# Performance work log

Measured on AMD Instinct MI355X. Metric: run time of the kernel, lower is better.

## Reference

```python
import jax, jax.numpy as jnp
import numpy as np

V = 50000
E = 640000
DIM = 128
NUM_EDGE_TYPES = 32


def setup_inputs() -> dict:
    key = jax.random.key(0)
    ks = jax.random.split(key, 8)
    return {
        "node_values": jax.random.normal(ks[0], (V, DIM), dtype=jnp.float32),
        "edge_src": jax.random.randint(ks[1], (E,), 0, V, dtype=jnp.int32),
        "edge_dest": jax.random.randint(ks[2], (E,), 0, V, dtype=jnp.int32),
        "edge_cls": jax.random.randint(ks[3], (E,), 0, NUM_EDGE_TYPES, dtype=jnp.int32),
        "W_src": jax.random.normal(ks[4], (DIM, DIM), dtype=jnp.float32) / np.sqrt(DIM),
        "b_src": jnp.zeros((DIM,), dtype=jnp.float32),
        "W_dest": jax.random.normal(ks[5], (DIM, DIM), dtype=jnp.float32) / np.sqrt(DIM),
        "b_dest": jnp.zeros((DIM,), dtype=jnp.float32),
        "edge_emb": jax.random.normal(ks[6], (NUM_EDGE_TYPES, DIM), dtype=jnp.float32),
    }


def reference(node_values, edge_src, edge_dest, edge_cls, W_src, b_src, W_dest, b_dest, edge_emb):
    # Dense projections over all nodes, then gather per edge (matches tf.gather(dense(...), idx))
    src_proj = node_values @ W_src + b_src    # [V, dim]
    dest_proj = node_values @ W_dest + b_dest  # [V, dim]
    # Per-edge fused message: gather src, gather dest, edge-class embedding lookup, add, relu
    msgs = jax.nn.relu(src_proj[edge_src] + dest_proj[edge_dest] + edge_emb[edge_cls])  # [E, dim]
    # Scatter-reduce messages onto destination nodes
    out = jax.ops.segment_sum(msgs, edge_dest, num_segments=V)  # [V, dim]
    return out
```

## Files before the change

### kernel.cpp

```cpp
#include <hip/hip_runtime.h>


#define V 50000
#define E 640000
#define DIM 128
#define NXCD 8
#define DRANGE 6250
#define NBIN_R 50
#define BINW 125
#define BINCAP 2048
#define NCHUNK 256
#define EC4 625
#define NE_MAX 512
#define QCAP 384
#define NPROJ 782

typedef __bf16 bf16x8 __attribute__((ext_vector_type(8)));
typedef float  f32x4  __attribute__((ext_vector_type(4)));
typedef float  f32x2  __attribute__((ext_vector_type(2)));

__device__ __forceinline__ float bf2f(unsigned int u16) {
    union { unsigned int i; float f; } c; c.i = u16 << 16; return c.f;
}
__device__ __forceinline__ unsigned int f2bf(float f) {
    union { float f; unsigned int i; } c; c.f = f;
    unsigned int u = c.i;
    return (u + 0x7FFFu + ((u >> 16) & 1u)) >> 16;
}

__global__ __launch_bounds__(256) void mp_setup(
    const float* __restrict__ Ws, const float* __restrict__ Wd,
    const float* __restrict__ emb,
    unsigned short* __restrict__ Wpk, unsigned short* __restrict__ embB,
    int* __restrict__ binCnt)
{
    int tid = blockIdx.x * 256 + threadIdx.x;
    int mat  = tid >> 11;
    int rem  = tid & 2047;
    int ct   = rem >> 8;
    int kt   = (rem >> 6) & 3;
    int lane = rem & 63;
    const float* W = mat ? Wd : Ws;
    int n  = ct * 16 + (lane & 15);
    int k0 = kt * 32 + (lane >> 4) * 8;
    unsigned short* dst = Wpk + (size_t)tid * 8;
    #pragma unroll
    for (int j = 0; j < 8; ++j) dst[j] = (unsigned short)f2bf(W[(k0 + j) * DIM + n]);
    embB[tid] = (unsigned short)f2bf(emb[tid]);
    if (tid < NXCD * NBIN_R) binCnt[tid] = 0;
}

__global__ __launch_bounds__(256) void mp_fused(
    const int* __restrict__ ed, const int* __restrict__ es, const int* __restrict__ ec,
    int* __restrict__ binCnt, int* __restrict__ binbuf,
    const float* __restrict__ x, const unsigned short* __restrict__ Wpk,
    const float* __restrict__ bs, const float* __restrict__ bd,
    unsigned char* __restrict__ ps8, unsigned short* __restrict__ pdB)
{
    __shared__ int ebuf[NE_MAX];
    __shared__ unsigned char bbin[NE_MAX];
    __shared__ int csr[NE_MAX];
    __shared__ unsigned char sbin[NE_MAX];
    __shared__ int hist[NBIN_R];
    __shared__ int lofs[NBIN_R + 1];
    __shared__ int lcur[NBIN_R];
    __shared__ int gbase[NBIN_R];
    __shared__ int ecnt;
    __shared__ float stage[4][16 * 132];

    const int b = blockIdx.x;
    const int role = b % 3;
    const int t = threadIdx.x;

    if (role != 2) {
        const int chunk = (b / 3) * 2 + role;
        const int r = chunk & (NXCD - 1);
        const int c = chunk >> 3;
        const int dlo = r * DRANGE;

        if (t < NBIN_R) hist[t] = 0;
        if (t == 0) ecnt = 0;
        __syncthreads();

        int4 DV[3], SV[3], CV[3];
        {
            const int4* ed4 = (const int4*)ed + c * EC4;
            const int4* es4 = (const int4*)es + c * EC4;
            const int4* ec4 = (const int4*)ec + c * EC4;
            #pragma unroll
            for (int k = 0; k < 3; ++k) {
                int i = t + k * 256;
                if (i < EC4) { DV[k] = ed4[i]; SV[k] = es4[i]; CV[k] = ec4[i]; }
                else { DV[k] = make_int4(-1, -1, -1, -1);
                       SV[k] = make_int4(0, 0, 0, 0); CV[k] = make_int4(0, 0, 0, 0); }
            }
        }

        #pragma unroll
        for (int k = 0; k < 3; ++k) {
            #define PUSH(D, S, C) { \
                int rel = (D) - dlo; \
                if ((unsigned)rel < DRANGE) { \
                    int bin = (unsigned)rel / BINW; \
                    int rl  = rel - bin * BINW; \
                    atomicAdd(&hist[bin], 1); \
                    int pos = atomicAdd(&ecnt, 1); \
                    if (pos < NE_MAX) { \
                        ebuf[pos] = ((S) & 0xFFFF) | ((C) << 16) | (rl << 21); \
                        bbin[pos] = (unsigned char)bin; \
                    } } }
            PUSH(DV[k].x, SV[k].x, CV[k].x); PUSH(DV[k].y, SV[k].y, CV[k].y);
            PUSH(DV[k].z, SV[k].z, CV[k].z); PUSH(DV[k].w, SV[k].w, CV[k].w);
            #undef PUSH
        }
        __syncthreads();

        if (t < NBIN_R) gbase[t] = atomicAdd(&binCnt[r * NBIN_R + t], hist[t]);
        if (t < 64) {
            int v = (t < NBIN_R) ? hist[t] : 0;
            #pragma unroll
            for (int dlt = 1; dlt < 64; dlt <<= 1) {
                int u = __shfl_up(v, dlt, 64);
                if (t >= dlt) v += u;
            }
            if (t < NBIN_R) { lofs[t + 1] = v; lcur[t] = v - hist[t]; }
            if (t == 0) lofs[0] = 0;
        }
        __syncthreads();

        int ne = ecnt; if (ne > NE_MAX) ne = NE_MAX;

        for (int i = t; i < ne; i += 256) {
            int bb = bbin[i];
            int p = atomicAdd(&lcur[bb], 1);
            csr[p] = ebuf[i];
            sbin[p] = (unsigned char)bb;
        }
        __syncthreads();

        for (int i = t; i < ne; i += 256) {
            int bb = sbin[i];
            int slot = gbase[bb] + (i - lofs[bb]);
            if (slot < BINCAP)
                binbuf[(r * NBIN_R + bb) * BINCAP + slot] = csr[i];
        }
        return;
    }

    const int p = b / 3;
    if (p >= NPROJ) return;
    const int wave = __builtin_amdgcn_readfirstlane(threadIdx.x) >> 6;
    const int lane = threadIdx.x & 63;
    const int m = lane & 15, q = lane >> 4;
    const int row0 = p * 64 + wave * 16;

    int arow = row0 + m; if (arow >= V) arow = V - 1;
    const float* xr = x + (size_t)arow * DIM + q * 8;

    bf16x8 A[4];
    #pragma unroll
    for (int kt = 0; kt < 4; ++kt) {
        float4 u = *(const float4*)(xr + kt * 32);
        float4 v = *(const float4*)(xr + kt * 32 + 4);
        bf16x8 a;
        a[0] = (__bf16)u.x; a[1] = (__bf16)u.y; a[2] = (__bf16)u.z; a[3] = (__bf16)u.w;
        a[4] = (__bf16)v.x; a[5] = (__bf16)v.y; a[6] = (__bf16)v.z; a[7] = (__bf16)v.w;
        A[kt] = a;
    }

    const bf16x8* Bp = (const bf16x8*)Wpk;

    f32x4 accS[8], accD[8];
    #pragma unroll
    for (int ct = 0; ct < 8; ++ct) {
        f32x4 aS = {0.f, 0.f, 0.f, 0.f}, aD = {0.f, 0.f, 0.f, 0.f};
        #pragma unroll
        for (int kt = 0; kt < 4; ++kt) {
            bf16x8 bS = Bp[((0 * 8 + ct) * 4 + kt) * 64 + lane];
            bf16x8 bD = Bp[((1 * 8 + ct) * 4 + kt) * 64 + lane];
            aS = __builtin_amdgcn_mfma_f32_16x16x32_bf16(A[kt], bS, aS, 0, 0, 0);
            aD = __builtin_amdgcn_mfma_f32_16x16x32_bf16(A[kt], bD, aD, 0, 0, 0);
        }
        accS[ct] = aS; accD[ct] = aD;
    }

    float* st = stage[wave];
    const int rr = lane & 15, cg = lane >> 4;
    const int orow = row0 + rr;
    const float* rowp = st + rr * 132 + cg * 32;

    #pragma unroll
    for (int ct = 0; ct < 8; ++ct) {
        const float bv = bs[ct * 16 + m];
        #pragma unroll
        for (int rg = 0; rg < 4; ++rg)
            st[(q * 4 + rg) * 132 + ct * 16 + m] = accS[ct][rg] + bv;
    }
    __syncthreads();
    {
        int w[8];
        #pragma unroll
        for (int j = 0; j < 8; ++j) {
            float4 f = *(const float4*)(rowp + 4 * j);
            int v = __builtin_amdgcn_cvt_pk_fp8_f32(f.x, f.y, 0, false);
            v = __builtin_amdgcn_cvt_pk_fp8_f32(f.z, f.w, v, true);
            w[j] = v;
        }
        if (orow < V) {
            int4* dst = (int4*)(ps8 + (size_t)orow * 128 + cg * 32);
            dst[0] = make_int4(w[0], w[1], w[2], w[3]);
            dst[1] = make_int4(w[4], w[5], w[6], w[7]);
        }
    }
    __syncthreads();

    #pragma unroll
    for (int ct = 0; ct < 8; ++ct) {
        const float bv = bd[ct * 16 + m];
        #pragma unroll
        for (int rg = 0; rg < 4; ++rg)
            st[(q * 4 + rg) * 132 + ct * 16 + m] = accD[ct][rg] + bv;
    }
    __syncthreads();
    {
        int w[16];
        #pragma unroll
        for (int j = 0; j < 8; ++j) {
            float4 f = *(const float4*)(rowp + 4 * j);
            w[2 * j]     = f2bf(f.x) | (f2bf(f.y) << 16);
            w[2 * j + 1] = f2bf(f.z) | (f2bf(f.w) << 16);
        }
        if (orow < V) {
            int4* dst = (int4*)(pdB + (size_t)orow * 128 + cg * 32);
            #pragma unroll
            for (int jj = 0; jj < 4; ++jj)
                dst[jj] = make_int4(w[4 * jj], w[4 * jj + 1], w[4 * jj + 2], w[4 * jj + 3]);
        }
    }
}

__global__ __launch_bounds__(256) void mp_binBC(
    const unsigned char* __restrict__ ps8, const unsigned short* __restrict__ pdB,
    const unsigned short* __restrict__ embB,
    const int* __restrict__ binCnt, const int* __restrict__ binbuf,
    float* __restrict__ out)
{
    __shared__ int csr[QCAP];
    __shared__ int cnt[16];
    __shared__ int off[17];
    __shared__ int cur[16];

    const int r = blockIdx.x & (NXCD - 1);
    const int rest = blockIdx.x >> 3;
    const int bi = rest % NBIN_R;
    const int qu = rest / NBIN_R;
    const int bin = r * NBIN_R + bi;
    const int rel0 = qu * 16;
    const int relW = (qu == 7) ? 13 : 16;
    const int d0 = bin * BINW + rel0;
    const int t = threadIdx.x;
    const int wave = t >> 6, lane = t & 63;

    int nb = binCnt[bin]; if (nb > BINCAP) nb = BINCAP;
    const int* buf = binbuf + (size_t)bin * BINCAP;

    if (t < 16) cnt[t] = 0;

    int EB[8];
    #pragma unroll
    for (int k = 0; k < 8; ++k) {
        int i = t + k * 256;
        EB[k] = (i < nb) ? buf[i] : -1;
    }

    float dp0v[4], dp1v[4];
    #pragma unroll
    for (int k = 0; k < 4; ++k) {
        int rl = wave + k * 4;
        int d = d0 + ((rl < relW) ? rl : 0);
        unsigned int pdu = *(const unsigned int*)(pdB + (size_t)d * DIM + 2 * lane);
        dp0v[k] = bf2f(pdu & 0xFFFF); dp1v[k] = bf2f(pdu >> 16);
    }
    __syncthreads();

    #pragma unroll
    for (int k = 0; k < 8; ++k) {
        int rl = (int)((unsigned)EB[k] >> 21) - rel0;
        if ((unsigned)rl < (unsigned)relW) atomicAdd(&cnt[rl], 1);
    }
    __syncthreads();

    if (t < 16) {
        int v = (t < relW) ? cnt[t] : 0;
        #pragma unroll
        for (int dlt = 1; dlt < 16; dlt <<= 1) {
            int u = __shfl_up(v, dlt, 64);
            if (t >= dlt) v += u;
        }
        off[t + 1] = v;
        cur[t] = v - cnt[t];
        if (t == 0) off[0] = 0;
    }
    __syncthreads();

    #pragma unroll
    for (int k = 0; k < 8; ++k) {
        int rl = (int)((unsigned)EB[k] >> 21) - rel0;
        if ((unsigned)rl < (unsigned)relW) {
            int pos = atomicAdd(&cur[rl], 1);
            if (pos < QCAP) csr[pos] = EB[k];
        }
    }
    __syncthreads();

    #define PROC(P) { \
        int s_ = *(const unsigned short*)(ps8 + ((size_t)((P) & 0xFFFF) << 7) + 2 * lane); \
        unsigned int e_ = *(const unsigned int*)(embB + ((((P) >> 16) & 0x1F) << 7) + 2 * lane); \
        f32x2 f_ = __builtin_amdgcn_cvt_pk_f32_fp8(s_, false); \
        a0 += fmaxf(f_.x + dp0 + bf2f(e_ & 0xFFFF), 0.f); \
        a1 += fmaxf(f_.y + dp1 + bf2f(e_ >> 16),    0.f); }

    #pragma unroll
    for (int k = 0; k < 4; ++k) {
        const int rl = wave + k * 4;
        if (rl >= relW) break;
        const int d = d0 + rl;
        int i0 = off[rl], i1 = off[rl + 1];
        if (i1 > QCAP) i1 = QCAP;
        if (i0 > i1) i0 = i1;
        const float dp0 = dp0v[k], dp1 = dp1v[k];
        float a0 = 0.f, a1 = 0.f;
        int i = i0;
        for (; i + 8 <= i1; i += 8) {
            int p0 = csr[i],     p1 = csr[i + 1], p2 = csr[i + 2], p3 = csr[i + 3];
            int p4 = csr[i + 4], p5 = csr[i + 5], p6 = csr[i + 6], p7 = csr[i + 7];
            PROC(p0); PROC(p1); PROC(p2); PROC(p3);
            PROC(p4); PROC(p5); PROC(p6); PROC(p7);
        }
        for (; i + 4 <= i1; i += 4) {
            int p0 = csr[i], p1 = csr[i + 1], p2 = csr[i + 2], p3 = csr[i + 3];
            PROC(p0); PROC(p1); PROC(p2); PROC(p3);
        }
        for (; i < i1; ++i) { int p0 = csr[i]; PROC(p0); }
        *(float2*)(out + (size_t)d * DIM + 2 * lane) = make_float2(a0, a1);
    }
    #undef PROC
}

extern "C" void kernel_launch(void* const* d_in, const int* in_sizes, int n_in,
                              void* d_out, int out_size, void* d_ws, size_t ws_size,
                              hipStream_t stream) {
    const float* x   = (const float*)d_in[0];
    const int*   es  = (const int*)d_in[1];
    const int*   ed  = (const int*)d_in[2];
    const int*   ec  = (const int*)d_in[3];
    const float* Ws  = (const float*)d_in[4];
    const float* bs  = (const float*)d_in[5];
    const float* Wd  = (const float*)d_in[6];
    const float* bd  = (const float*)d_in[7];
    const float* emb = (const float*)d_in[8];
    float* out = (float*)d_out;

    char* ws = (char*)d_ws;
    size_t off = 0;
    unsigned char*  ps8  = (unsigned char*)(ws + off);  off += (size_t)V * 128;
    unsigned short* pdB  = (unsigned short*)(ws + off); off += (size_t)V * DIM * 2;
    int* binbuf = (int*)(ws + off);                     off += (size_t)400 * BINCAP * 4;
    int* binCnt = (int*)(ws + off);                     off += 400 * 4;
    unsigned short* Wpk  = (unsigned short*)(ws + off); off += 2 * 128 * 128 * 2;
    unsigned short* embB = (unsigned short*)(ws + off); off += 32 * 128 * 2;

    mp_setup<<<16, 256, 0, stream>>>(Ws, Wd, emb, Wpk, embB, binCnt);
    mp_fused<<<3072, 256, 0, stream>>>(ed, es, ec, binCnt, binbuf,
                                       x, Wpk, bs, bd, ps8, pdB);
    mp_binBC<<<NBIN_R * NXCD * 8, 256, 0, stream>>>(ps8, pdB, embB, binCnt, binbuf, out);
}
```

Baseline: 146.5 us.

## Replace per-XCD coarse binning with single-pass fine 16-node destination bins

Edge binning now uses 3125 global bins of 16 destination nodes each. Each edge chunk is read once and placed with a local histogram plus one global atomic reservation per bin, instead of being re-read by 8 per-XCD blocks and compacted through shared memory. The consumer kernel launches one block per fine bin and reads at most 384 entries instead of filtering 2048-entry coarse bins; the edge-embedding table is staged in LDS. In exchange it issues many more global atomics and uncoalesced single-int scatter writes, and it relies on no bin exceeding 384 edges.

```diff
diff --git a/kernel.cpp b/kernel.cpp
--- a/kernel.cpp
+++ b/kernel.cpp
@@ -4,16 +4,12 @@
 #define V 50000
 #define E 640000
 #define DIM 128
-#define NXCD 8
-#define DRANGE 6250
-#define NBIN_R 50
-#define BINW 125
-#define BINCAP 2048
+#define NBIN_F 3125
+#define QCAP 384
 #define NCHUNK 256
 #define EC4 625
-#define NE_MAX 512
-#define QCAP 384
 #define NPROJ 782
+#define NFUSED 1038
 
 typedef __bf16 bf16x8 __attribute__((ext_vector_type(8)));
 typedef float  f32x4  __attribute__((ext_vector_type(4)));
@@ -47,7 +43,7 @@
     #pragma unroll
     for (int j = 0; j < 8; ++j) dst[j] = (unsigned short)f2bf(W[(k0 + j) * DIM + n]);
     embB[tid] = (unsigned short)f2bf(emb[tid]);
-    if (tid < NXCD * NBIN_R) binCnt[tid] = 0;
+    if (tid < NBIN_F) binCnt[tid] = 0;
 }
 
 __global__ __launch_bounds__(256) void mp_fused(
@@ -57,36 +53,22 @@
     const float* __restrict__ bs, const float* __restrict__ bd,
     unsigned char* __restrict__ ps8, unsigned short* __restrict__ pdB)
 {
-    __shared__ int ebuf[NE_MAX];
-    __shared__ unsigned char bbin[NE_MAX];
-    __shared__ int csr[NE_MAX];
-    __shared__ unsigned char sbin[NE_MAX];
-    __shared__ int hist[NBIN_R];
-    __shared__ int lofs[NBIN_R + 1];
-    __shared__ int lcur[NBIN_R];
-    __shared__ int gbase[NBIN_R];
-    __shared__ int ecnt;
     __shared__ float stage[4][16 * 132];
 
     const int b = blockIdx.x;
-    const int role = b % 3;
     const int t = threadIdx.x;
-
-    if (role != 2) {
-        const int chunk = (b / 3) * 2 + role;
-        const int r = chunk & (NXCD - 1);
-        const int c = chunk >> 3;
-        const int dlo = r * DRANGE;
-
-        if (t < NBIN_R) hist[t] = 0;
-        if (t == 0) ecnt = 0;
-        __syncthreads();
+    const bool isBin = ((b & 3) == 3) && (b < 1024);
+
+    if (isBin) {
+        int* cnt = (int*)&stage[0][0];
+        const int c = b >> 2;
+        for (int i = t; i < NBIN_F; i += 256) cnt[i] = 0;
 
         int4 DV[3], SV[3], CV[3];
         {
-            const int4* ed4 = (const int4*)ed + c * EC4;
-            const int4* es4 = (const int4*)es + c * EC4;
-            const int4* ec4 = (const int4*)ec + c * EC4;
+            const int4* ed4 = (const int4*)ed + (size_t)c * EC4;
+            const int4* es4 = (const int4*)es + (size_t)c * EC4;
+            const int4* ec4 = (const int4*)ec + (size_t)c * EC4;
             #pragma unroll
             for (int k = 0; k < 3; ++k) {
                 int i = t + k * 256;
@@ -95,59 +77,38 @@
                        SV[k] = make_int4(0, 0, 0, 0); CV[k] = make_int4(0, 0, 0, 0); }
             }
         }
+        __syncthreads();
 
         #pragma unroll
         for (int k = 0; k < 3; ++k) {
-            #define PUSH(D, S, C) { \
-                int rel = (D) - dlo; \
-                if ((unsigned)rel < DRANGE) { \
-                    int bin = (unsigned)rel / BINW; \
-                    int rl  = rel - bin * BINW; \
-                    atomicAdd(&hist[bin], 1); \
-                    int pos = atomicAdd(&ecnt, 1); \
-                    if (pos < NE_MAX) { \
-                        ebuf[pos] = ((S) & 0xFFFF) | ((C) << 16) | (rl << 21); \
-                        bbin[pos] = (unsigned char)bin; \
-                    } } }
-            PUSH(DV[k].x, SV[k].x, CV[k].x); PUSH(DV[k].y, SV[k].y, CV[k].y);
-            PUSH(DV[k].z, SV[k].z, CV[k].z); PUSH(DV[k].w, SV[k].w, CV[k].w);
-            #undef PUSH
+            #define H1(D) if ((D) >= 0) atomicAdd(&cnt[(unsigned)(D) >> 4], 1);
+            H1(DV[k].x); H1(DV[k].y); H1(DV[k].z); H1(DV[k].w);
+            #undef H1
         }
         __syncthreads();
 
-        if (t < NBIN_R) gbase[t] = atomicAdd(&binCnt[r * NBIN_R + t], hist[t]);
-        if (t < 64) {
-            int v = (t < NBIN_R) ? hist[t] : 0;
-            #pragma unroll
-            for (int dlt = 1; dlt < 64; dlt <<= 1) {
-                int u = __shfl_up(v, dlt, 64);
-                if (t >= dlt) v += u;
-            }
-            if (t < NBIN_R) { lofs[t + 1] = v; lcur[t] = v - hist[t]; }
-            if (t == 0) lofs[0] = 0;
+        for (int i = t; i < NBIN_F; i += 256) {
+            int c0 = cnt[i];
+            if (c0) cnt[i] = atomicAdd(&binCnt[i], c0);
         }
         __syncthreads();
 
-        int ne = ecnt; if (ne > NE_MAX) ne = NE_MAX;
-
-        for (int i = t; i < ne; i += 256) {
-            int bb = bbin[i];
-            int p = atomicAdd(&lcur[bb], 1);
-            csr[p] = ebuf[i];
-            sbin[p] = (unsigned char)bb;
-        }
-        __syncthreads();
-
-        for (int i = t; i < ne; i += 256) {
-            int bb = sbin[i];
-            int slot = gbase[bb] + (i - lofs[bb]);
-            if (slot < BINCAP)
-                binbuf[(r * NBIN_R + bb) * BINCAP + slot] = csr[i];
+        #pragma unroll
+        for (int k = 0; k < 3; ++k) {
+            #define SC1(D, S, C) if ((D) >= 0) { \
+                int bn = (unsigned)(D) >> 4; \
+                int sl = atomicAdd(&cnt[bn], 1); \
+                if (sl < QCAP) \
+                    binbuf[(size_t)bn * QCAP + sl] = \
+                        ((S) & 0xFFFF) | ((C) << 16) | (((D) & 15) << 21); }
+            SC1(DV[k].x, SV[k].x, CV[k].x); SC1(DV[k].y, SV[k].y, CV[k].y);
+            SC1(DV[k].z, SV[k].z, CV[k].z); SC1(DV[k].w, SV[k].w, CV[k].w);
+            #undef SC1
         }
         return;
     }
 
-    const int p = b / 3;
+    const int p = b - ((b < 1024) ? ((b + 1) >> 2) : 256);
     if (p >= NPROJ) return;
     const int wave = __builtin_amdgcn_readfirstlane(threadIdx.x) >> 6;
     const int lane = threadIdx.x & 63;
@@ -249,49 +210,47 @@
     __shared__ int cnt[16];
     __shared__ int off[17];
     __shared__ int cur[16];
-
-    const int r = blockIdx.x & (NXCD - 1);
-    const int rest = blockIdx.x >> 3;
-    const int bi = rest % NBIN_R;
-    const int qu = rest / NBIN_R;
-    const int bin = r * NBIN_R + bi;
-    const int rel0 = qu * 16;
-    const int relW = (qu == 7) ? 13 : 16;
-    const int d0 = bin * BINW + rel0;
+    __shared__ unsigned short sEmb[32 * DIM];
+
+    const int bin = blockIdx.x;
+    const int d0 = bin << 4;
     const int t = threadIdx.x;
     const int wave = t >> 6, lane = t & 63;
 
-    int nb = binCnt[bin]; if (nb > BINCAP) nb = BINCAP;
-    const int* buf = binbuf + (size_t)bin * BINCAP;
+    int nb = binCnt[bin]; if (nb > QCAP) nb = QCAP;
+    const int* buf = binbuf + (size_t)bin * QCAP;
 
     if (t < 16) cnt[t] = 0;
 
-    int EB[8];
-    #pragma unroll
-    for (int k = 0; k < 8; ++k) {
-        int i = t + k * 256;
-        EB[k] = (i < nb) ? buf[i] : -1;
-    }
+    {
+        const int4* s4 = (const int4*)embB;
+        int4* d4 = (int4*)sEmb;
+        d4[t] = s4[t];
+        d4[t + 256] = s4[t + 256];
+    }
+
+    int EB[2];
+    EB[0] = (t < nb) ? buf[t] : -1;
+    EB[1] = (t + 256 < nb) ? buf[t + 256] : -1;
 
     float dp0v[4], dp1v[4];
     #pragma unroll
     for (int k = 0; k < 4; ++k) {
-        int rl = wave + k * 4;
-        int d = d0 + ((rl < relW) ? rl : 0);
+        int d = d0 + wave + k * 4;
         unsigned int pdu = *(const unsigned int*)(pdB + (size_t)d * DIM + 2 * lane);
         dp0v[k] = bf2f(pdu & 0xFFFF); dp1v[k] = bf2f(pdu >> 16);
     }
     __syncthreads();
 
     #pragma unroll
-    for (int k = 0; k < 8; ++k) {
-        int rl = (int)((unsigned)EB[k] >> 21) - rel0;
-        if ((unsigned)rl < (unsigned)relW) atomicAdd(&cnt[rl], 1);
+    for (int k = 0; k < 2; ++k) {
+        unsigned int rl = (unsigned)EB[k] >> 21;
+        if (rl < 16u) atomicAdd(&cnt[rl], 1);
     }
     __syncthreads();
 
     if (t < 16) {
-        int v = (t < relW) ? cnt[t] : 0;
+        int v = cnt[t];
         #pragma unroll
         for (int dlt = 1; dlt < 16; dlt <<= 1) {
             int u = __shfl_up(v, dlt, 64);
@@ -304,18 +263,18 @@
     __syncthreads();
 
     #pragma unroll
-    for (int k = 0; k < 8; ++k) {
-        int rl = (int)((unsigned)EB[k] >> 21) - rel0;
-        if ((unsigned)rl < (unsigned)relW) {
+    for (int k = 0; k < 2; ++k) {
+        unsigned int rl = (unsigned)EB[k] >> 21;
+        if (rl < 16u) {
             int pos = atomicAdd(&cur[rl], 1);
-            if (pos < QCAP) csr[pos] = EB[k];
+            csr[pos] = EB[k];
         }
     }
     __syncthreads();
 
     #define PROC(P) { \
         int s_ = *(const unsigned short*)(ps8 + ((size_t)((P) & 0xFFFF) << 7) + 2 * lane); \
-        unsigned int e_ = *(const unsigned int*)(embB + ((((P) >> 16) & 0x1F) << 7) + 2 * lane); \
+        unsigned int e_ = *(const unsigned int*)(sEmb + ((((P) >> 16) & 0x1F) << 7) + 2 * lane); \
         f32x2 f_ = __builtin_amdgcn_cvt_pk_f32_fp8(s_, false); \
         a0 += fmaxf(f_.x + dp0 + bf2f(e_ & 0xFFFF), 0.f); \
         a1 += fmaxf(f_.y + dp1 + bf2f(e_ >> 16),    0.f); }
@@ -323,11 +282,8 @@
     #pragma unroll
     for (int k = 0; k < 4; ++k) {
         const int rl = wave + k * 4;
-        if (rl >= relW) break;
         const int d = d0 + rl;
         int i0 = off[rl], i1 = off[rl + 1];
-        if (i1 > QCAP) i1 = QCAP;
-        if (i0 > i1) i0 = i1;
         const float dp0 = dp0v[k], dp1 = dp1v[k];
         float a0 = 0.f, a1 = 0.f;
         int i = i0;
@@ -365,13 +321,13 @@
     size_t off = 0;
     unsigned char*  ps8  = (unsigned char*)(ws + off);  off += (size_t)V * 128;
     unsigned short* pdB  = (unsigned short*)(ws + off); off += (size_t)V * DIM * 2;
-    int* binbuf = (int*)(ws + off);                     off += (size_t)400 * BINCAP * 4;
-    int* binCnt = (int*)(ws + off);                     off += 400 * 4;
+    int* binbuf = (int*)(ws + off);                     off += (size_t)NBIN_F * QCAP * 4;
+    int* binCnt = (int*)(ws + off);                     off += (size_t)NBIN_F * 4;
     unsigned short* Wpk  = (unsigned short*)(ws + off); off += 2 * 128 * 128 * 2;
     unsigned short* embB = (unsigned short*)(ws + off); off += 32 * 128 * 2;
 
     mp_setup<<<16, 256, 0, stream>>>(Ws, Wd, emb, Wpk, embB, binCnt);
-    mp_fused<<<3072, 256, 0, stream>>>(ed, es, ec, binCnt, binbuf,
-                                       x, Wpk, bs, bd, ps8, pdB);
-    mp_binBC<<<NBIN_R * NXCD * 8, 256, 0, stream>>>(ps8, pdB, embB, binCnt, binbuf, out);
-}
+    mp_fused<<<NFUSED, 256, 0, stream>>>(ed, es, ec, binCnt, binbuf,
+                                         x, Wpk, bs, bd, ps8, pdB);
+    mp_binBC<<<NBIN_F, 256, 0, stream>>>(ps8, pdB, embB, binCnt, binbuf, out);
+}
```

New measurement: 158.6 us. 8.3% more time.

## Partition edges into 4 destination ranges and bin with two-pass counting sort

Applied to the files above, without the earlier changes.

Edge partitioning now uses 4 destination ranges of 100 bins each instead of 8 ranges of 50, so each chunk is read by 4 blocks rather than 8, which halves redundant index reads. The binning pass becomes a histogram followed by a direct scatter into CSR order held in registers, removing the global ecnt atomic and an intermediate shared buffer. Shared memory now reuses the projection staging array. The binBC kernel caches the edge-class embedding table in LDS. The block mix and interleave of binning and projection blocks is also changed. The risk is that a larger NE_MAX and longer scans could overflow caps.

```diff
diff --git a/kernel.cpp b/kernel.cpp
--- a/kernel.cpp
+++ b/kernel.cpp
@@ -4,16 +4,18 @@
 #define V 50000
 #define E 640000
 #define DIM 128
-#define NXCD 8
-#define DRANGE 6250
-#define NBIN_R 50
+#define NRES 4
+#define DRANGE 12500
+#define NBIN_R 100
 #define BINW 125
+#define NBINS 400
 #define BINCAP 2048
+#define NE_MAX 896
+#define QCAP 384
 #define NCHUNK 256
 #define EC4 625
-#define NE_MAX 512
-#define QCAP 384
 #define NPROJ 782
+#define NFUSED 1806
 
 typedef __bf16 bf16x8 __attribute__((ext_vector_type(8)));
 typedef float  f32x4  __attribute__((ext_vector_type(4)));
@@ -47,7 +49,7 @@
     #pragma unroll
     for (int j = 0; j < 8; ++j) dst[j] = (unsigned short)f2bf(W[(k0 + j) * DIM + n]);
     embB[tid] = (unsigned short)f2bf(emb[tid]);
-    if (tid < NXCD * NBIN_R) binCnt[tid] = 0;
+    if (tid < NBINS) binCnt[tid] = 0;
 }
 
 __global__ __launch_bounds__(256) void mp_fused(
@@ -57,36 +59,33 @@
     const float* __restrict__ bs, const float* __restrict__ bd,
     unsigned char* __restrict__ ps8, unsigned short* __restrict__ pdB)
 {
-    __shared__ int ebuf[NE_MAX];
-    __shared__ unsigned char bbin[NE_MAX];
-    __shared__ int csr[NE_MAX];
-    __shared__ unsigned char sbin[NE_MAX];
-    __shared__ int hist[NBIN_R];
-    __shared__ int lofs[NBIN_R + 1];
-    __shared__ int lcur[NBIN_R];
-    __shared__ int gbase[NBIN_R];
-    __shared__ int ecnt;
     __shared__ float stage[4][16 * 132];
 
     const int b = blockIdx.x;
-    const int role = b % 3;
     const int t = threadIdx.x;
-
-    if (role != 2) {
-        const int chunk = (b / 3) * 2 + role;
-        const int r = chunk & (NXCD - 1);
-        const int c = chunk >> 3;
+    const int r7 = b % 7;
+    const bool isBin = (b < 1792) && (r7 < 4);
+
+    if (isBin) {
+        int* hist  = (int*)&stage[0][0];
+        int* lofs  = hist + NBIN_R;
+        int* lcur  = lofs + NBIN_R + 1;
+        int* gbase = lcur + NBIN_R;
+        int* csr   = gbase + NBIN_R;
+        unsigned short* sbin = (unsigned short*)(csr + NE_MAX);
+
+        const int a = (b / 7) * 4 + r7;
+        const int r = a & (NRES - 1);
+        const int c = a >> 2;
         const int dlo = r * DRANGE;
 
         if (t < NBIN_R) hist[t] = 0;
-        if (t == 0) ecnt = 0;
-        __syncthreads();
 
         int4 DV[3], SV[3], CV[3];
         {
-            const int4* ed4 = (const int4*)ed + c * EC4;
-            const int4* es4 = (const int4*)es + c * EC4;
-            const int4* ec4 = (const int4*)ec + c * EC4;
+            const int4* ed4 = (const int4*)ed + (size_t)c * EC4;
+            const int4* es4 = (const int4*)es + (size_t)c * EC4;
+            const int4* ec4 = (const int4*)ec + (size_t)c * EC4;
             #pragma unroll
             for (int k = 0; k < 3; ++k) {
                 int i = t + k * 256;
@@ -95,59 +94,66 @@
                        SV[k] = make_int4(0, 0, 0, 0); CV[k] = make_int4(0, 0, 0, 0); }
             }
         }
+        __syncthreads();
 
         #pragma unroll
         for (int k = 0; k < 3; ++k) {
-            #define PUSH(D, S, C) { \
-                int rel = (D) - dlo; \
-                if ((unsigned)rel < DRANGE) { \
-                    int bin = (unsigned)rel / BINW; \
-                    int rl  = rel - bin * BINW; \
-                    atomicAdd(&hist[bin], 1); \
-                    int pos = atomicAdd(&ecnt, 1); \
-                    if (pos < NE_MAX) { \
-                        ebuf[pos] = ((S) & 0xFFFF) | ((C) << 16) | (rl << 21); \
-                        bbin[pos] = (unsigned char)bin; \
-                    } } }
-            PUSH(DV[k].x, SV[k].x, CV[k].x); PUSH(DV[k].y, SV[k].y, CV[k].y);
-            PUSH(DV[k].z, SV[k].z, CV[k].z); PUSH(DV[k].w, SV[k].w, CV[k].w);
-            #undef PUSH
+            #define H1(D) { int rel = (D) - dlo; \
+                if ((unsigned)rel < DRANGE) atomicAdd(&hist[(unsigned)rel / BINW], 1); }
+            H1(DV[k].x); H1(DV[k].y); H1(DV[k].z); H1(DV[k].w);
+            #undef H1
         }
         __syncthreads();
 
         if (t < NBIN_R) gbase[t] = atomicAdd(&binCnt[r * NBIN_R + t], hist[t]);
         if (t < 64) {
-            int v = (t < NBIN_R) ? hist[t] : 0;
+            int carry = 0;
             #pragma unroll
-            for (int dlt = 1; dlt < 64; dlt <<= 1) {
-                int u = __shfl_up(v, dlt, 64);
-                if (t >= dlt) v += u;
+            for (int s = 0; s < 2; ++s) {
+                int idx = s * 64 + t;
+                int v = (idx < NBIN_R) ? hist[idx] : 0;
+                #pragma unroll
+                for (int dlt = 1; dlt < 64; dlt <<= 1) {
+                    int u = __shfl_up(v, dlt, 64);
+                    if (t >= dlt) v += u;
+                }
+                int tot = __shfl(v, 63, 64);
+                v += carry;
+                if (idx < NBIN_R) { lofs[idx + 1] = v; lcur[idx] = v - hist[idx]; }
+                carry += tot;
             }
-            if (t < NBIN_R) { lofs[t + 1] = v; lcur[t] = v - hist[t]; }
             if (t == 0) lofs[0] = 0;
         }
         __syncthreads();
 
-        int ne = ecnt; if (ne > NE_MAX) ne = NE_MAX;
-
-        for (int i = t; i < ne; i += 256) {
-            int bb = bbin[i];
-            int p = atomicAdd(&lcur[bb], 1);
-            csr[p] = ebuf[i];
-            sbin[p] = (unsigned char)bb;
+        #pragma unroll
+        for (int k = 0; k < 3; ++k) {
+            #define SC1(D, S, C) { int rel = (D) - dlo; \
+                if ((unsigned)rel < DRANGE) { \
+                    int bn = (unsigned)rel / BINW; \
+                    int rl = rel - bn * BINW; \
+                    int pos = atomicAdd(&lcur[bn], 1); \
+                    if (pos < NE_MAX) { \
+                        csr[pos] = ((S) & 0xFFFF) | ((C) << 16) | (rl << 21); \
+                        sbin[pos] = (unsigned short)bn; } } }
+            SC1(DV[k].x, SV[k].x, CV[k].x); SC1(DV[k].y, SV[k].y, CV[k].y);
+            SC1(DV[k].z, SV[k].z, CV[k].z); SC1(DV[k].w, SV[k].w, CV[k].w);
+            #undef SC1
         }
         __syncthreads();
+
+        int ne = lofs[NBIN_R]; if (ne > NE_MAX) ne = NE_MAX;
 
         for (int i = t; i < ne; i += 256) {
             int bb = sbin[i];
             int slot = gbase[bb] + (i - lofs[bb]);
             if (slot < BINCAP)
-                binbuf[(r * NBIN_R + bb) * BINCAP + slot] = csr[i];
+                binbuf[(size_t)(r * NBIN_R + bb) * BINCAP + slot] = csr[i];
         }
         return;
     }
 
-    const int p = b / 3;
+    const int p = (b < 1792) ? ((b / 7) * 3 + (r7 - 4)) : (768 + (b - 1792));
     if (p >= NPROJ) return;
     const int wave = __builtin_amdgcn_readfirstlane(threadIdx.x) >> 6;
     const int lane = threadIdx.x & 63;
@@ -249,12 +255,10 @@
     __shared__ int cnt[16];
     __shared__ int off[17];
     __shared__ int cur[16];
-
-    const int r = blockIdx.x & (NXCD - 1);
-    const int rest = blockIdx.x >> 3;
-    const int bi = rest % NBIN_R;
-    const int qu = rest / NBIN_R;
-    const int bin = r * NBIN_R + bi;
+    __shared__ unsigned short sEmb[32 * DIM];
+
+    const int bin = blockIdx.x >> 3;
+    const int qu = blockIdx.x & 7;
     const int rel0 = qu * 16;
     const int relW = (qu == 7) ? 13 : 16;
     const int d0 = bin * BINW + rel0;
@@ -266,6 +270,13 @@
 
     if (t < 16) cnt[t] = 0;
 
+    {
+        const int4* s4 = (const int4*)embB;
+        int4* d4 = (int4*)sEmb;
+        d4[t] = s4[t];
+        d4[t + 256] = s4[t + 256];
+    }
+
     int EB[8];
     #pragma unroll
     for (int k = 0; k < 8; ++k) {
@@ -315,7 +326,7 @@
 
     #define PROC(P) { \
         int s_ = *(const unsigned short*)(ps8 + ((size_t)((P) & 0xFFFF) << 7) + 2 * lane); \
-        unsigned int e_ = *(const unsigned int*)(embB + ((((P) >> 16) & 0x1F) << 7) + 2 * lane); \
+        unsigned int e_ = *(const unsigned int*)(sEmb + ((((P) >> 16) & 0x1F) << 7) + 2 * lane); \
         f32x2 f_ = __builtin_amdgcn_cvt_pk_f32_fp8(s_, false); \
         a0 += fmaxf(f_.x + dp0 + bf2f(e_ & 0xFFFF), 0.f); \
         a1 += fmaxf(f_.y + dp1 + bf2f(e_ >> 16),    0.f); }
@@ -365,13 +376,13 @@
     size_t off = 0;
     unsigned char*  ps8  = (unsigned char*)(ws + off);  off += (size_t)V * 128;
     unsigned short* pdB  = (unsigned short*)(ws + off); off += (size_t)V * DIM * 2;
-    int* binbuf = (int*)(ws + off);                     off += (size_t)400 * BINCAP * 4;
-    int* binCnt = (int*)(ws + off);                     off += 400 * 4;
+    int* binbuf = (int*)(ws + off);                     off += (size_t)NBINS * BINCAP * 4;
+    int* binCnt = (int*)(ws + off);                     off += (size_t)NBINS * 4;
     unsigned short* Wpk  = (unsigned short*)(ws + off); off += 2 * 128 * 128 * 2;
     unsigned short* embB = (unsigned short*)(ws + off); off += 32 * 128 * 2;
 
     mp_setup<<<16, 256, 0, stream>>>(Ws, Wd, emb, Wpk, embB, binCnt);
-    mp_fused<<<3072, 256, 0, stream>>>(ed, es, ec, binCnt, binbuf,
-                                       x, Wpk, bs, bd, ps8, pdB);
-    mp_binBC<<<NBIN_R * NXCD * 8, 256, 0, stream>>>(ps8, pdB, embB, binCnt, binbuf, out);
-}
+    mp_fused<<<NFUSED, 256, 0, stream>>>(ed, es, ec, binCnt, binbuf,
+                                         x, Wpk, bs, bd, ps8, pdB);
+    mp_binBC<<<NBINS * 8, 256, 0, stream>>>(ps8, pdB, embB, binCnt, binbuf, out);
+}
```

Measured after the change: 155.0 us. 1.06x slower.
